# Optimization experiments

Hardware: AMD Instinct MI355X
Metric: run time of the kernel (lower is better)

Reference implementation:

```python
import jax, jax.numpy as jnp
import numpy as np

EPS = 1e-12

def _pairwise_dist(a, b):
    # a: [B,N,3], b: [B,M,3] -> Euclidean distances [B,N,M]
    d2 = (jnp.sum(a * a, -1)[:, :, None]
          + jnp.sum(b * b, -1)[:, None, :]
          - 2.0 * jnp.einsum('bnd,bmd->bnm', a, b))
    return jnp.sqrt(jnp.maximum(d2, EPS))


def setup_inputs() -> dict:
    key = jax.random.key(0)
    k1, k2, k3 = jax.random.split(key, 3)
    B, N, M = 16, 4096, 1024
    shape_xyz = jax.random.normal(k1, (B, N, 6), dtype=jnp.float32)
    skel_xyz = jax.random.normal(k2, (B, M, 3), dtype=jnp.float32)
    skel_nori = jax.random.normal(k3, (B, M, 3), dtype=jnp.float32)
    return {"shape_xyz": shape_xyz, "skel_xyz": skel_xyz, "skel_nori": skel_nori}


def reference(shape_xyz, skel_xyz, skel_nori):
    normal = shape_xyz[:, :, 3:6]          # [B,N,3]
    pts = shape_xyz[:, :, :3]              # [B,N,3]
    B = skel_nori.shape[0]

    # Chamfer-style closest distances (sum of min Euclidean distances, both ways)
    d_shape2skel = _pairwise_dist(pts, skel_xyz)   # [B,N,M]
    cd1 = jnp.sum(jnp.min(d_shape2skel, axis=2))
    cd2 = jnp.sum(jnp.min(d_shape2skel, axis=1))   # same matrix transposed
    loss_cd = (cd1 + cd2) * 0.0001

    # KNN (k=2) of each skeletal point among shape points (cKDTree equivalent)
    d_skel2shape = jnp.transpose(d_shape2skel, (0, 2, 1))  # [B,M,N]
    _, idx = jax.lax.top_k(-d_skel2shape, 2)               # [B,M,2]

    # Gather normals of the 2 nearest shape points: [B,M,2,3]
    knn_normals = jnp.take_along_axis(normal[:, None, :, :],
                                      idx[:, :, :, None], axis=2)
    dots = jnp.einsum('bmd,bmkd->bmk', skel_nori, knn_normals)  # [B,M,2]
    # |dot| averaged over k, summed over (b, j), divided by batch size
    loss_normal = jnp.sum(jnp.mean(jnp.abs(dots), axis=-1)) / B

    return loss_cd + 0.001 * loss_normal
```

## Files before the change

### kernel.cpp

```cpp
#include <hip/hip_runtime.h>
#include <cfloat>
#include <stdint.h>

#define B_ 16
#define N_ 4096
#define M_ 1024
#define EPS_ 1e-12f

typedef float v2f __attribute__((ext_vector_type(2)));

__device__ __forceinline__ v2f fma2(v2f a, v2f b, v2f c) {
    return __builtin_elementwise_fma(a, b, c);
}
__device__ __forceinline__ v2f splat(float x) { return (v2f){x, x}; }

__device__ __forceinline__ uint32_t umin3(uint32_t a, uint32_t b, uint32_t c) {
    return min(a, min(b, c));
}
__device__ __forceinline__ uint32_t umed3(uint32_t a, uint32_t b, uint32_t c) {
    return max(min(a, b), min(max(a, b), c));
}

__global__ __launch_bounds__(256, 3) void fused_kernel(const float* __restrict__ shape_xyz,
                                                       const float* __restrict__ skel_xyz,
                                                       const float* __restrict__ skel_nori,
                                                       float* __restrict__ out)
{
    __shared__ float ls[8192];
    __shared__ float ws[4];

    const int tid = threadIdx.x;
    float4* A4 = (float4*)ls;
    float4* Bq = (float4*)(ls + 4096);
    float v = 0.0f;

    if (blockIdx.x < 256) {
        const int b    = blockIdx.x >> 4;
        const int tile = blockIdx.x & 15;

        const float4* g4 = (const float4*)(skel_xyz + (size_t)b * M_ * 3);
        const float4 r0 = g4[3 * tid + 0];
        const float4 r1 = g4[3 * tid + 1];
        const float4 r2 = g4[3 * tid + 2];

        const int sA = tid & 15;
        const int gA = tid >> 4;
        const int n0 = tile * 256 + gA * 16;
        const float* p = shape_xyz + ((size_t)b * N_ + n0) * 6;
        float nx[16], ny[16], nz[16], best[16];
#pragma unroll
        for (int k = 0; k < 16; ++k) {
            nx[k] = -p[k * 6 + 0];
            ny[k] = -p[k * 6 + 1];
            nz[k] = -p[k * 6 + 2];
            best[k] = FLT_MAX;
        }

        {
            const float w0 = fmaf(r0.x, r0.x, fmaf(r0.y, r0.y, r0.z * r0.z));
            const float w1 = fmaf(r0.w, r0.w, fmaf(r1.x, r1.x, r1.y * r1.y));
            const float w2 = fmaf(r1.z, r1.z, fmaf(r1.w, r1.w, r2.x * r2.x));
            const float w3 = fmaf(r2.y, r2.y, fmaf(r2.z, r2.z, r2.w * r2.w));
            A4[2 * tid + 0] = make_float4(2*r0.x, 2*r0.w, 2*r0.y, 2*r1.x);
            Bq[2 * tid + 0] = make_float4(2*r0.z, 2*r1.y, w0, w1);
            A4[2 * tid + 1] = make_float4(2*r1.z, 2*r2.y, 2*r1.w, 2*r2.z);
            Bq[2 * tid + 1] = make_float4(2*r2.x, 2*r2.w, w2, w3);
        }
        __syncthreads();

#pragma unroll 4
        for (int j = 0; j < 32; ++j) {
            const float4 a = A4[j * 16 + sA];
            const float4 bq = Bq[j * 16 + sA];
            const v2f sx = {a.x, a.y};
            const v2f sy = {a.z, a.w};
            const v2f sz = {bq.x, bq.y};
            const v2f sw = {bq.z, bq.w};
#pragma unroll
            for (int k = 0; k < 16; ++k) {
                const v2f t = fma2(splat(nx[k]), sx,
                              fma2(splat(ny[k]), sy,
                              fma2(splat(nz[k]), sz, sw)));
                best[k] = fminf(best[k], fminf(t.x, t.y));
            }
        }

#pragma unroll
        for (int off = 1; off < 16; off <<= 1) {
#pragma unroll
            for (int k = 0; k < 16; ++k) best[k] = fminf(best[k], __shfl_xor(best[k], off));
        }
        if (sA == 0) {
#pragma unroll
            for (int k = 0; k < 16; ++k) {
                const float pp = fmaf(nx[k], nx[k], fmaf(ny[k], ny[k], nz[k] * nz[k]));
                v += sqrtf(fmaxf(best[k] + pp, EPS_));
            }
            v *= 1e-4f;
        }
    } else {
        const int id  = blockIdx.x - 256;
        const int b   = id >> 5;
        const int sub = id & 31;
        const int s   = tid & 63;
        const int g   = tid >> 6;
        const int m0  = sub * 32 + g * 8;

        float m2x[8], m2y[8], m2z[8], aa[8];
        uint32_t k1[8], k2[8];
        {
            const float* sq = skel_xyz + ((size_t)b * M_ + m0) * 3;
#pragma unroll
            for (int c = 0; c < 8; ++c) {
                const float x = sq[c * 3 + 0];
                const float y = sq[c * 3 + 1];
                const float z = sq[c * 3 + 2];
                m2x[c] = -2.0f * x; m2y[c] = -2.0f * y; m2z[c] = -2.0f * z;
                aa[c]  = fmaf(x, x, fmaf(y, y, z * z));
                k1[c] = 0xFFFFFFFFu; k2[c] = 0xFFFFFFFFu;
            }
        }
        float amax = fmaxf(fmaxf(fmaxf(aa[0], aa[1]), fmaxf(aa[2], aa[3])),
                           fmaxf(fmaxf(aa[4], aa[5]), fmaxf(aa[6], aa[7])));
#pragma unroll
        for (int off = 1; off < 64; off <<= 1) amax = fmaxf(amax, __shfl_xor(amax, off));
        if ((tid & 63) == 0) ws[tid >> 6] = amax;

        const uint32_t HI = 0xFFFFF000u;
        const float* sb = shape_xyz + (size_t)b * N_ * 6;
        const float4* g4 = (const float4*)sb;

        float4 r[12];
#pragma unroll
        for (int k = 0; k < 12; ++k) r[k] = g4[12 * tid + k];

        float C = 0.0f;
        for (int ph = 0; ph < 2; ++ph) {
            __syncthreads();
            if (ph == 0) C = fmaxf(fmaxf(ws[0], ws[1]), fmaxf(ws[2], ws[3]));
#pragma unroll
            for (int h = 0; h < 2; ++h) {
                const float4 a0 = r[6 * h + 0], a1 = r[6 * h + 1], a2 = r[6 * h + 2];
                const float4 a3 = r[6 * h + 3], a4 = r[6 * h + 4], a5 = r[6 * h + 5];
                const float w0 = fmaf(a0.x, a0.x, fmaf(a0.y, a0.y, a0.z * a0.z)) + C;
                const float w1 = fmaf(a1.z, a1.z, fmaf(a1.w, a1.w, a2.x * a2.x)) + C;
                const float w2 = fmaf(a3.x, a3.x, fmaf(a3.y, a3.y, a3.z * a3.z)) + C;
                const float w3 = fmaf(a4.z, a4.z, fmaf(a4.w, a4.w, a5.x * a5.x)) + C;
                A4[4 * tid + 2 * h + 0] = make_float4(a0.x, a1.z, a0.y, a1.w);
                Bq[4 * tid + 2 * h + 0] = make_float4(a0.z, a2.x, w0, w1);
                A4[4 * tid + 2 * h + 1] = make_float4(a3.x, a4.z, a3.y, a4.w);
                Bq[4 * tid + 2 * h + 1] = make_float4(a3.z, a5.x, w2, w3);
            }
            __syncthreads();
            if (ph == 0) {
#pragma unroll
                for (int k = 0; k < 12; ++k) r[k] = g4[3072 + 12 * tid + k];
            }
            const uint32_t nb = (uint32_t)(ph * 2048);

#pragma unroll 2
            for (int j = 0; j < 16; ++j) {
                const float4 a = A4[j * 64 + s];
                const float4 bq = Bq[j * 64 + s];
                const v2f qx = {a.x, a.y};
                const v2f qy = {a.z, a.w};
                const v2f qz = {bq.x, bq.y};
                const v2f qw = {bq.z, bq.w};
                const uint32_t gn0 = nb + (uint32_t)(j * 128 + 2 * s);
                const uint32_t gn1 = gn0 + 1u;
#pragma unroll
                for (int c = 0; c < 8; ++c) {
                    const v2f t = fma2(splat(m2x[c]), qx,
                                  fma2(splat(m2y[c]), qy,
                                  fma2(splat(m2z[c]), qz, qw)));
                    const uint32_t kk0 = (__float_as_uint(t.x) & HI) | gn0;
                    const uint32_t kk1 = (__float_as_uint(t.y) & HI) | gn1;
                    k2[c] = min(k2[c], umed3(k1[c], kk0, kk1));
                    k1[c] = umin3(k1[c], kk0, kk1);
                }
            }
        }

#pragma unroll
        for (int off = 1; off < 64; off <<= 1) {
#pragma unroll
            for (int c = 0; c < 8; ++c) {
                const uint32_t o1 = (uint32_t)__shfl_xor((int)k1[c], off);
                const uint32_t o2 = (uint32_t)__shfl_xor((int)k2[c], off);
                const uint32_t nk2 = min(min(k2[c], o2), max(k1[c], o1));
                k1[c] = min(k1[c], o1);
                k2[c] = nk2;
            }
        }

        if (s == 0) {
            const float* no = skel_nori + ((size_t)b * M_ + m0) * 3;
            const float kN = 0.001f * 0.5f / (float)B_;
#pragma unroll
            for (int c = 0; c < 8; ++c) {
                const int i1 = (int)(k1[c] & 0xFFFu);
                const int i2 = (int)(k2[c] & 0xFFFu);
                const float* p1 = sb + (size_t)i1 * 6;
                const float* p2 = sb + (size_t)i2 * 6;
                const float ax = -0.5f * m2x[c], ay = -0.5f * m2y[c], az = -0.5f * m2z[c];
                const float dx = ax - p1[0], dy = ay - p1[1], dz = az - p1[2];
                const float d2 = fmaf(dx, dx, fmaf(dy, dy, dz * dz));
                const float q0 = no[c * 3 + 0], q1 = no[c * 3 + 1], q2 = no[c * 3 + 2];
                const float dot1 = q0 * p1[3] + q1 * p1[4] + q2 * p1[5];
                const float dot2 = q0 * p2[3] + q1 * p2[4] + q2 * p2[5];
                v += sqrtf(fmaxf(d2, EPS_)) * 1e-4f + (fabsf(dot1) + fabsf(dot2)) * kN;
            }
        }
    }

#pragma unroll
    for (int off = 32; off > 0; off >>= 1) v += __shfl_down(v, off);
    __syncthreads();
    if ((tid & 63) == 0) ws[tid >> 6] = v;
    __syncthreads();
    if (tid == 0) atomicAdd(out, ws[0] + ws[1] + ws[2] + ws[3]);
}

extern "C" void kernel_launch(void* const* d_in, const int* in_sizes, int n_in,
                              void* d_out, int out_size, void* d_ws, size_t ws_size,
                              hipStream_t stream) {
    const float* shape_xyz = (const float*)d_in[0];
    const float* skel_xyz  = (const float*)d_in[1];
    const float* skel_nori = (const float*)d_in[2];
    float* out = (float*)d_out;

    hipMemsetAsync(out, 0, sizeof(float), stream);
    fused_kernel<<<768, 256, 0, stream>>>(shape_xyz, skel_xyz, skel_nori, out);
}
```

Before: 82.63 us.

## Split KNN shape-point range across four blocks and merge in finalize kernel

```diff
diff --git a/kernel.cpp b/kernel.cpp
--- a/kernel.cpp
+++ b/kernel.cpp
@@ -21,18 +21,17 @@
     return max(min(a, b), min(max(a, b), c));
 }
 
-__global__ __launch_bounds__(256, 3) void fused_kernel(const float* __restrict__ shape_xyz,
+__global__ __launch_bounds__(256, 4) void fused_kernel(const float* __restrict__ shape_xyz,
                                                        const float* __restrict__ skel_xyz,
-                                                       const float* __restrict__ skel_nori,
+                                                       uint32_t* __restrict__ ws_out,
                                                        float* __restrict__ out)
 {
-    __shared__ float ls[8192];
-    __shared__ float ws[4];
+    __shared__ float ls[4096];
+    __shared__ float ws2[4];
 
     const int tid = threadIdx.x;
     float4* A4 = (float4*)ls;
-    float4* Bq = (float4*)(ls + 4096);
-    float v = 0.0f;
+    float4* Bq = (float4*)(ls + 2048);
 
     if (blockIdx.x < 256) {
         const int b    = blockIdx.x >> 4;
@@ -90,6 +89,7 @@
 #pragma unroll
             for (int k = 0; k < 16; ++k) best[k] = fminf(best[k], __shfl_xor(best[k], off));
         }
+        float v = 0.0f;
         if (sA == 0) {
 #pragma unroll
             for (int k = 0; k < 16; ++k) {
@@ -98,13 +98,20 @@
             }
             v *= 1e-4f;
         }
+#pragma unroll
+        for (int off = 32; off > 0; off >>= 1) v += __shfl_down(v, off);
+        if ((tid & 63) == 0) ws2[tid >> 6] = v;
+        __syncthreads();
+        if (tid == 0) atomicAdd(out, ws2[0] + ws2[1] + ws2[2] + ws2[3]);
     } else {
         const int id  = blockIdx.x - 256;
-        const int b   = id >> 5;
-        const int sub = id & 31;
+        const int b   = id >> 7;
+        const int sub = id & 127;
+        const int mc  = sub >> 2;
+        const int pc  = sub & 3;
         const int s   = tid & 63;
         const int g   = tid >> 6;
-        const int m0  = sub * 32 + g * 8;
+        const int m0  = mc * 32 + g * 8;
 
         float m2x[8], m2y[8], m2z[8], aa[8];
         uint32_t k1[8], k2[8];
@@ -124,60 +131,49 @@
                            fmaxf(fmaxf(aa[4], aa[5]), fmaxf(aa[6], aa[7])));
 #pragma unroll
         for (int off = 1; off < 64; off <<= 1) amax = fmaxf(amax, __shfl_xor(amax, off));
-        if ((tid & 63) == 0) ws[tid >> 6] = amax;
-
-        const uint32_t HI = 0xFFFFF000u;
+        if (s == 0) ws2[g] = amax;
+
         const float* sb = shape_xyz + (size_t)b * N_ * 6;
         const float4* g4 = (const float4*)sb;
-
-        float4 r[12];
-#pragma unroll
-        for (int k = 0; k < 12; ++k) r[k] = g4[12 * tid + k];
-
-        float C = 0.0f;
-        for (int ph = 0; ph < 2; ++ph) {
-            __syncthreads();
-            if (ph == 0) C = fmaxf(fmaxf(ws[0], ws[1]), fmaxf(ws[2], ws[3]));
-#pragma unroll
-            for (int h = 0; h < 2; ++h) {
-                const float4 a0 = r[6 * h + 0], a1 = r[6 * h + 1], a2 = r[6 * h + 2];
-                const float4 a3 = r[6 * h + 3], a4 = r[6 * h + 4], a5 = r[6 * h + 5];
-                const float w0 = fmaf(a0.x, a0.x, fmaf(a0.y, a0.y, a0.z * a0.z)) + C;
-                const float w1 = fmaf(a1.z, a1.z, fmaf(a1.w, a1.w, a2.x * a2.x)) + C;
-                const float w2 = fmaf(a3.x, a3.x, fmaf(a3.y, a3.y, a3.z * a3.z)) + C;
-                const float w3 = fmaf(a4.z, a4.z, fmaf(a4.w, a4.w, a5.x * a5.x)) + C;
-                A4[4 * tid + 2 * h + 0] = make_float4(a0.x, a1.z, a0.y, a1.w);
-                Bq[4 * tid + 2 * h + 0] = make_float4(a0.z, a2.x, w0, w1);
-                A4[4 * tid + 2 * h + 1] = make_float4(a3.x, a4.z, a3.y, a4.w);
-                Bq[4 * tid + 2 * h + 1] = make_float4(a3.z, a5.x, w2, w3);
-            }
-            __syncthreads();
-            if (ph == 0) {
-#pragma unroll
-                for (int k = 0; k < 12; ++k) r[k] = g4[3072 + 12 * tid + k];
-            }
-            const uint32_t nb = (uint32_t)(ph * 2048);
-
-#pragma unroll 2
-            for (int j = 0; j < 16; ++j) {
-                const float4 a = A4[j * 64 + s];
-                const float4 bq = Bq[j * 64 + s];
-                const v2f qx = {a.x, a.y};
-                const v2f qy = {a.z, a.w};
-                const v2f qz = {bq.x, bq.y};
-                const v2f qw = {bq.z, bq.w};
-                const uint32_t gn0 = nb + (uint32_t)(j * 128 + 2 * s);
-                const uint32_t gn1 = gn0 + 1u;
-#pragma unroll
-                for (int c = 0; c < 8; ++c) {
-                    const v2f t = fma2(splat(m2x[c]), qx,
-                                  fma2(splat(m2y[c]), qy,
-                                  fma2(splat(m2z[c]), qz, qw)));
-                    const uint32_t kk0 = (__float_as_uint(t.x) & HI) | gn0;
-                    const uint32_t kk1 = (__float_as_uint(t.y) & HI) | gn1;
-                    k2[c] = min(k2[c], umed3(k1[c], kk0, kk1));
-                    k1[c] = umin3(k1[c], kk0, kk1);
-                }
+        float4 r[6];
+#pragma unroll
+        for (int k = 0; k < 6; ++k) r[k] = g4[pc * 1536 + 6 * tid + k];
+        {
+            const float4 a0 = r[0], a1 = r[1], a2 = r[2];
+            const float4 a3 = r[3], a4 = r[4], a5 = r[5];
+            const float w0 = fmaf(a0.x, a0.x, fmaf(a0.y, a0.y, a0.z * a0.z));
+            const float w1 = fmaf(a1.z, a1.z, fmaf(a1.w, a1.w, a2.x * a2.x));
+            const float w2 = fmaf(a3.x, a3.x, fmaf(a3.y, a3.y, a3.z * a3.z));
+            const float w3 = fmaf(a4.z, a4.z, fmaf(a4.w, a4.w, a5.x * a5.x));
+            A4[2 * tid + 0] = make_float4(a0.x, a1.z, a0.y, a1.w);
+            Bq[2 * tid + 0] = make_float4(a0.z, a2.x, w0, w1);
+            A4[2 * tid + 1] = make_float4(a3.x, a4.z, a3.y, a4.w);
+            Bq[2 * tid + 1] = make_float4(a3.z, a5.x, w2, w3);
+        }
+        __syncthreads();
+        const float C = fmaxf(fmaxf(ws2[0], ws2[1]), fmaxf(ws2[2], ws2[3]));
+        const uint32_t HI = 0xFFFFF000u;
+        const uint32_t nbase = (uint32_t)(pc * 1024 + 2 * s);
+
+#pragma unroll
+        for (int j = 0; j < 8; ++j) {
+            const float4 a = A4[j * 64 + s];
+            const float4 bq = Bq[j * 64 + s];
+            const v2f qx = {a.x, a.y};
+            const v2f qy = {a.z, a.w};
+            const v2f qz = {bq.x, bq.y};
+            const v2f qw0 = {bq.z + C, bq.w + C};
+            const uint32_t gn0 = nbase + (uint32_t)(j * 128);
+            const uint32_t gn1 = gn0 + 1u;
+#pragma unroll
+            for (int c = 0; c < 8; ++c) {
+                const v2f t = fma2(splat(m2x[c]), qx,
+                              fma2(splat(m2y[c]), qy,
+                              fma2(splat(m2z[c]), qz, qw0)));
+                const uint32_t kk0 = (__float_as_uint(t.x) & HI) | gn0;
+                const uint32_t kk1 = (__float_as_uint(t.y) & HI) | gn1;
+                k2[c] = min(k2[c], umed3(k1[c], kk0, kk1));
+                k1[c] = umin3(k1[c], kk0, kk1);
             }
         }
 
@@ -194,31 +190,54 @@
         }
 
         if (s == 0) {
-            const float* no = skel_nori + ((size_t)b * M_ + m0) * 3;
-            const float kN = 0.001f * 0.5f / (float)B_;
-#pragma unroll
-            for (int c = 0; c < 8; ++c) {
-                const int i1 = (int)(k1[c] & 0xFFFu);
-                const int i2 = (int)(k2[c] & 0xFFFu);
-                const float* p1 = sb + (size_t)i1 * 6;
-                const float* p2 = sb + (size_t)i2 * 6;
-                const float ax = -0.5f * m2x[c], ay = -0.5f * m2y[c], az = -0.5f * m2z[c];
-                const float dx = ax - p1[0], dy = ay - p1[1], dz = az - p1[2];
-                const float d2 = fmaf(dx, dx, fmaf(dy, dy, dz * dz));
-                const float q0 = no[c * 3 + 0], q1 = no[c * 3 + 1], q2 = no[c * 3 + 2];
-                const float dot1 = q0 * p1[3] + q1 * p1[4] + q2 * p1[5];
-                const float dot2 = q0 * p2[3] + q1 * p2[4] + q2 * p2[5];
-                v += sqrtf(fmaxf(d2, EPS_)) * 1e-4f + (fabsf(dot1) + fabsf(dot2)) * kN;
-            }
+            uint2* w2 = (uint2*)ws_out;
+#pragma unroll
+            for (int c = 0; c < 8; ++c)
+                w2[(size_t)((b << 10) + m0 + c) * 4 + pc] = make_uint2(k1[c], k2[c]);
         }
     }
+}
+
+__global__ __launch_bounds__(256, 8) void finalize_kernel(const float* __restrict__ shape_xyz,
+                                                          const float* __restrict__ skel_xyz,
+                                                          const float* __restrict__ skel_nori,
+                                                          const uint32_t* __restrict__ ws_in,
+                                                          float* __restrict__ out)
+{
+    __shared__ float red[4];
+    const int tid = threadIdx.x;
+    const int gm  = blockIdx.x * 256 + tid;
+    const int b   = gm >> 10;
+
+    const uint2* w2 = (const uint2*)ws_in;
+    uint32_t K1v = 0xFFFFFFFFu, K2v = 0xFFFFFFFFu;
+#pragma unroll
+    for (int pcn = 0; pcn < 4; ++pcn) {
+        const uint2 pr = w2[(size_t)gm * 4 + pcn];
+        K2v = min(K2v, umed3(K1v, pr.x, pr.y));
+        K1v = umin3(K1v, pr.x, pr.y);
+    }
+
+    const float* sb = shape_xyz + (size_t)b * N_ * 6;
+    const int i1 = (int)(K1v & 0xFFFu);
+    const int i2 = (int)(K2v & 0xFFFu);
+    const float* p1 = sb + (size_t)i1 * 6;
+    const float* p2 = sb + (size_t)i2 * 6;
+    const float* sq = skel_xyz + (size_t)gm * 3;
+    const float* no = skel_nori + (size_t)gm * 3;
+    const float dx = sq[0] - p1[0], dy = sq[1] - p1[1], dz = sq[2] - p1[2];
+    const float d2 = fmaf(dx, dx, fmaf(dy, dy, dz * dz));
+    const float q0 = no[0], q1 = no[1], q2 = no[2];
+    const float dot1 = q0 * p1[3] + q1 * p1[4] + q2 * p1[5];
+    const float dot2 = q0 * p2[3] + q1 * p2[4] + q2 * p2[5];
+    const float kN = 0.001f * 0.5f / (float)B_;
+    float v = sqrtf(fmaxf(d2, EPS_)) * 1e-4f + (fabsf(dot1) + fabsf(dot2)) * kN;
 
 #pragma unroll
     for (int off = 32; off > 0; off >>= 1) v += __shfl_down(v, off);
+    if ((tid & 63) == 0) red[tid >> 6] = v;
     __syncthreads();
-    if ((tid & 63) == 0) ws[tid >> 6] = v;
-    __syncthreads();
-    if (tid == 0) atomicAdd(out, ws[0] + ws[1] + ws[2] + ws[3]);
+    if (tid == 0) atomicAdd(out, red[0] + red[1] + red[2] + red[3]);
 }
 
 extern "C" void kernel_launch(void* const* d_in, const int* in_sizes, int n_in,
@@ -228,7 +247,9 @@
     const float* skel_xyz  = (const float*)d_in[1];
     const float* skel_nori = (const float*)d_in[2];
     float* out = (float*)d_out;
+    uint32_t* ws = (uint32_t*)d_ws;
 
     hipMemsetAsync(out, 0, sizeof(float), stream);
-    fused_kernel<<<768, 256, 0, stream>>>(shape_xyz, skel_xyz, skel_nori, out);
-}
+    fused_kernel<<<2304, 256, 0, stream>>>(shape_xyz, skel_xyz, ws, out);
+    finalize_kernel<<<64, 256, 0, stream>>>(shape_xyz, skel_xyz, skel_nori, ws, out);
+}
```

Measured after the change: 112.2 us. 1.36x slower.
